# Kernel optimization log

Measured on AMD Instinct MI355X. Metric: run time of the kernel, lower is better.

Reference implementation:

```python
import jax, jax.numpy as jnp
import numpy as np


def _rmsnorm(x):
    # F.rms_norm with no weight, default eps = finfo(dtype).eps
    eps = jnp.asarray(jnp.finfo(x.dtype).eps, x.dtype)
    return x * jax.lax.rsqrt(jnp.mean(x * x, axis=-1, keepdims=True) + eps)


def _rope(x, cos, sin):
    d = x.shape[-1] // 2
    x1, x2 = x[..., :d], x[..., d:]
    return jnp.concatenate([x1 * cos + x2 * sin, -x1 * sin + x2 * cos], axis=-1)


def setup_inputs() -> dict:
    key = jax.random.key(0)
    ks = jax.random.split(key, 9)
    B, T, C, H, D = 4, 2048, 1024, 8, 128
    x = jax.random.normal(ks[0], (B, T, C), jnp.float32)
    ve = jax.random.normal(ks[1], (B, T, C), jnp.float32)
    cos = jax.random.uniform(ks[2], (1, T, 1, D // 2), jnp.float32)
    sin = jax.random.uniform(ks[3], (1, T, 1, D // 2), jnp.float32)
    s = 0.02
    Wq = jax.random.normal(ks[4], (C, C), jnp.float32) * s
    Wk = jax.random.normal(ks[5], (C, C), jnp.float32) * s
    Wv = jax.random.normal(ks[6], (C, C), jnp.float32) * s
    Wproj = jax.random.normal(ks[7], (C, C), jnp.float32) * s
    Wgate = jax.random.normal(ks[8], (H, 32), jnp.float32) * s
    return {"x": x, "ve": ve, "cos": cos, "sin": sin,
            "Wq": Wq, "Wk": Wk, "Wv": Wv, "Wproj": Wproj, "Wgate": Wgate,
            "window_size": 1024}


def reference(x, ve, cos, sin, Wq, Wk, Wv, Wproj, Wgate, window_size):
    B, T, C = x.shape
    H = Wgate.shape[0]
    D = C // H
    gate_ch = Wgate.shape[1]  # 32

    q = (x @ Wq.T).reshape(B, T, H, D)
    k = (x @ Wk.T).reshape(B, T, H, D)
    v = (x @ Wv.T).reshape(B, T, H, D)

    # value-embedding sigmoid gate: gate in (0, 2)
    gate = 2.0 * jax.nn.sigmoid(x[..., :gate_ch] @ Wgate.T)  # [B,T,H]
    v = v + gate[..., None] * ve.reshape(B, T, H, D)

    q = _rmsnorm(_rope(q, cos, sin))
    k = _rmsnorm(_rope(k, cos, sin))

    scale = jnp.asarray(D, q.dtype) ** -0.5
    scores = jnp.einsum("bqhd,bkhd->bhqk", q, k) * scale  # [B,H,T,T]

    pos = jnp.arange(T)
    row, col = pos[:, None], pos[None, :]
    mask = (col <= row) & (col >= row - window_size + 1)  # sliding causal window
    scores = jnp.where(mask, scores, -jnp.inf)
    attn = jax.nn.softmax(scores, axis=-1)

    y = jnp.einsum("bhqk,bkhd->bqhd", attn, v).reshape(B, T, C)
    return y @ Wproj.T
```

## Files before the change

### kernel.cpp

```cpp
#include <hip/hip_runtime.h>
#include <cstdint>
#include <cstddef>

typedef __bf16 bf16;
typedef __bf16 bf16x8 __attribute__((ext_vector_type(8)));
typedef float  f32x4  __attribute__((ext_vector_type(4)));

#define AS1 __attribute__((address_space(1)))
#define AS3 __attribute__((address_space(3)))

#define B_ 4
#define T_ 2048
#define C_ 1024
#define H_ 8
#define D_ 128
#define WIN_ 1024
#define PS_ 72

__global__ void cvt_kernel(const float* __restrict__ src, bf16* __restrict__ dst, int n) {
  int i = (blockIdx.x * 256 + threadIdx.x) * 8;
  if (i >= n) return;
  float4 a = *(const float4*)(src + i);
  float4 b = *(const float4*)(src + i + 4);
  bf16x8 o;
  o[0] = (bf16)a.x; o[1] = (bf16)a.y; o[2] = (bf16)a.z; o[3] = (bf16)a.w;
  o[4] = (bf16)b.x; o[5] = (bf16)b.y; o[6] = (bf16)b.z; o[7] = (bf16)b.w;
  *(bf16x8*)(dst + i) = o;
}

__device__ __forceinline__ void gemm_tile_compute(
    const bf16* __restrict__ A, const bf16* __restrict__ W,
    bf16* As, bf16* Bs, int m0, int n0, f32x4 acc[4][4])
{
  const int tid  = threadIdx.x;
  const int w    = tid >> 6;
  const int l    = tid & 63;
  const int quad = l >> 4;
  const int arow = l & 15;
  const int lrow = tid >> 3;
  const int lcol = ((tid & 7) ^ (lrow & 7)) * 8;
  const int wm = w >> 1, wn = w & 1;
  const int sw = (arow & 7);

  for (int kt = 0; kt < C_; kt += 64) {
    __syncthreads();
#pragma unroll
    for (int i = 0; i < 4; i++) {
      const bf16* ga = A + (size_t)(m0 + i * 32 + lrow) * C_ + kt + lcol;
      __builtin_amdgcn_global_load_lds((AS1 unsigned int*)ga,
          (AS3 unsigned int*)(As + i * 2048 + w * 512), 16, 0, 0);
      const bf16* gb = W + (size_t)(n0 + i * 32 + lrow) * C_ + kt + lcol;
      __builtin_amdgcn_global_load_lds((AS1 unsigned int*)gb,
          (AS3 unsigned int*)(Bs + i * 2048 + w * 512), 16, 0, 0);
    }
    __syncthreads();

#pragma unroll
    for (int ks = 0; ks < 2; ks++) {
      const int ch = ((ks * 4 + quad) ^ sw) * 8;
      bf16x8 af[4], bfr[4];
#pragma unroll
      for (int mt = 0; mt < 4; mt++)
        af[mt] = *(const bf16x8*)(As + (wm * 64 + mt * 16 + arow) * 64 + ch);
#pragma unroll
      for (int nt = 0; nt < 4; nt++)
        bfr[nt] = *(const bf16x8*)(Bs + (wn * 64 + nt * 16 + arow) * 64 + ch);
#pragma unroll
      for (int mt = 0; mt < 4; mt++)
#pragma unroll
        for (int nt = 0; nt < 4; nt++)
          acc[mt][nt] = __builtin_amdgcn_mfma_f32_16x16x32_bf16(af[mt], bfr[nt], acc[mt][nt], 0, 0, 0);
    }
  }
}

__global__ __launch_bounds__(256) void gemm_qkv(
    const bf16* __restrict__ xb, const bf16* __restrict__ wb,
    bf16* __restrict__ qh, bf16* __restrict__ kh, bf16* __restrict__ vh)
{
  __shared__ bf16 As[128 * 64];
  __shared__ bf16 Bs[128 * 64];
  const int z = blockIdx.z;
  const bf16* W = wb + (size_t)z * (C_ * C_);
  bf16* out = (z == 0) ? qh : (z == 1) ? kh : vh;
  const int m0 = blockIdx.y * 128, n0 = blockIdx.x * 128;

  f32x4 acc[4][4];
#pragma unroll
  for (int i = 0; i < 4; i++)
#pragma unroll
    for (int j = 0; j < 4; j++) acc[i][j] = (f32x4){0.f, 0.f, 0.f, 0.f};

  gemm_tile_compute(xb, W, As, Bs, m0, n0, acc);

  const int tid = threadIdx.x, w = tid >> 6, l = tid & 63;
  const int quad = l >> 4, lc = l & 15, wm = w >> 1, wn = w & 1;
#pragma unroll
  for (int mt = 0; mt < 4; mt++) {
#pragma unroll
    for (int nt = 0; nt < 4; nt++) {
      const int col = n0 + wn * 64 + nt * 16 + lc;
      const int h = col >> 7, d = col & 127;
#pragma unroll
      for (int r = 0; r < 4; r++) {
        const int row = m0 + wm * 64 + mt * 16 + quad * 4 + r;
        const int b = row >> 11, t = row & 2047;
        out[(((size_t)(b * H_ + h)) * T_ + t) * D_ + d] = (bf16)acc[mt][nt][r];
      }
    }
  }
}

__global__ __launch_bounds__(256) void gemm_proj(
    const bf16* __restrict__ yb, const bf16* __restrict__ wproj, float* __restrict__ out)
{
  __shared__ bf16 As[128 * 64];
  __shared__ bf16 Bs[128 * 64];
  const int m0 = blockIdx.y * 128, n0 = blockIdx.x * 128;

  f32x4 acc[4][4];
#pragma unroll
  for (int i = 0; i < 4; i++)
#pragma unroll
    for (int j = 0; j < 4; j++) acc[i][j] = (f32x4){0.f, 0.f, 0.f, 0.f};

  gemm_tile_compute(yb, wproj, As, Bs, m0, n0, acc);

  const int tid = threadIdx.x, w = tid >> 6, l = tid & 63;
  const int quad = l >> 4, lc = l & 15, wm = w >> 1, wn = w & 1;
#pragma unroll
  for (int mt = 0; mt < 4; mt++) {
#pragma unroll
    for (int nt = 0; nt < 4; nt++) {
      const int col = n0 + wn * 64 + nt * 16 + lc;
#pragma unroll
      for (int r = 0; r < 4; r++) {
        const int row = m0 + wm * 64 + mt * 16 + quad * 4 + r;
        out[(size_t)row * C_ + col] = acc[mt][nt][r];
      }
    }
  }
}

__global__ __launch_bounds__(256) void rope_rms_gate(
    bf16* __restrict__ qh, bf16* __restrict__ kh, bf16* __restrict__ vh,
    const float* __restrict__ x, const float* __restrict__ ve,
    const float* __restrict__ cosb, const float* __restrict__ sinb,
    const float* __restrict__ wg)
{
  const int tid = threadIdx.x, w = tid >> 6, l = tid & 63;
  const int rq = blockIdx.x * 4 + w;
  const int b = rq >> 14, h = (rq >> 11) & 7, t = rq & 2047;
  const float cv = cosb[t * 64 + l], sv = sinb[t * 64 + l];
  const float eps = 1.1920929e-07f;
  const float QSC = 0.08838834764831845f * 1.4426950408889634f;

  bf16* qr = qh + (size_t)rq * D_;
  float x1 = (float)qr[l], x2 = (float)qr[l + 64];
  float o1 = x1 * cv + x2 * sv;
  float o2 = x2 * cv - x1 * sv;
  float ss = o1 * o1 + o2 * o2;
#pragma unroll
  for (int off = 32; off; off >>= 1) ss += __shfl_xor(ss, off);
  float sc = rsqrtf(ss * (1.0f / 128.0f) + eps) * QSC;
  qr[l] = (bf16)(o1 * sc); qr[l + 64] = (bf16)(o2 * sc);

  bf16* kr = kh + (size_t)rq * D_;
  x1 = (float)kr[l]; x2 = (float)kr[l + 64];
  o1 = x1 * cv + x2 * sv;
  o2 = x2 * cv - x1 * sv;
  ss = o1 * o1 + o2 * o2;
#pragma unroll
  for (int off = 32; off; off >>= 1) ss += __shfl_xor(ss, off);
  sc = rsqrtf(ss * (1.0f / 128.0f) + eps);
  kr[l] = (bf16)(o1 * sc); kr[l + 64] = (bf16)(o2 * sc);

  const float* xr = x + ((size_t)(b * T_ + t)) * C_;
  float gp = (l < 32) ? xr[l] * wg[h * 32 + l] : 0.0f;
#pragma unroll
  for (int off = 32; off; off >>= 1) gp += __shfl_xor(gp, off);
  const float gate = 2.0f / (1.0f + __expf(-gp));
  bf16* vr = vh + (size_t)rq * D_;
  const float* ver = ve + ((size_t)(b * T_ + t)) * C_ + h * D_;
  vr[l]      = (bf16)((float)vr[l]      + gate * ver[l]);
  vr[l + 64] = (bf16)((float)vr[l + 64] + gate * ver[l + 64]);
}

__global__ __launch_bounds__(256) void transpose_v(
    const bf16* __restrict__ vh, bf16* __restrict__ vt)
{
  __shared__ float tile[64 * 65];
  const int bh = blockIdx.z;
  const int t0 = blockIdx.x * 64, d0 = blockIdx.y * 64;
  const int tid = threadIdx.x;
  const int r8 = tid >> 3, c8 = (tid & 7) * 8;
#pragma unroll
  for (int g = 0; g < 2; g++) {
    const int t = r8 + g * 32;
    bf16x8 v = *(const bf16x8*)(vh + ((size_t)bh * T_ + t0 + t) * D_ + d0 + c8);
#pragma unroll
    for (int j = 0; j < 8; j++) tile[t * 65 + c8 + j] = (float)v[j];
  }
  __syncthreads();
#pragma unroll
  for (int g = 0; g < 2; g++) {
    const int d = r8 + g * 32;
    bf16x8 o;
#pragma unroll
    for (int j = 0; j < 8; j++) o[j] = (bf16)tile[(c8 + j) * 65 + d];
    *(bf16x8*)(vt + ((size_t)bh * D_ + d0 + d) * T_ + t0 + c8) = o;
  }
}

__global__ __launch_bounds__(256) void attn_mfma(
    const bf16* __restrict__ qh, const bf16* __restrict__ kh,
    const bf16* __restrict__ vt, bf16* __restrict__ yb)
{
  __shared__ bf16 Ks[64 * 128];
  __shared__ bf16 VTs[128 * 64];
  __shared__ bf16 Ps[4 * 32 * PS_];
  const int bh = blockIdx.y;
  const int q0 = blockIdx.x * 128;
  const int tid = threadIdx.x;
  const int w = tid >> 6, l = tid & 63;
  const int quad = l >> 4, l15 = l & 15;
  const int sw = l15 & 7;
  const float FMAX = 16.5f;

  bf16x8 qf[2][4];
  const bf16* qbase = qh + ((size_t)bh * T_ + q0 + w * 32 + l15) * D_;
#pragma unroll
  for (int mt = 0; mt < 2; mt++)
#pragma unroll
    for (int dk = 0; dk < 4; dk++)
      qf[mt][dk] = *(const bf16x8*)(qbase + mt * 16 * D_ + dk * 32 + quad * 8);

  f32x4 O[2][8];
  f32x4 lst[2];
#pragma unroll
  for (int mt = 0; mt < 2; mt++) {
    lst[mt] = (f32x4){0.f, 0.f, 0.f, 0.f};
#pragma unroll
    for (int dn = 0; dn < 8; dn++) O[mt][dn] = (f32x4){0.f, 0.f, 0.f, 0.f};
  }

  const int kt_lo = (q0 >= WIN_) ? ((q0 - (WIN_ - 1)) >> 6) : 0;
  const int kt_hi = (q0 + 127) >> 6;
  const bf16* kg = kh + (size_t)bh * T_ * D_;
  const bf16* vg = vt + (size_t)bh * D_ * T_;
  bf16* Pw = Ps + w * 32 * PS_;

  const int krow_s = w * 4 + (l >> 4);
  const int kcol_s = (l15 ^ (krow_s & 7)) * 8;
  const int vrow_s = w * 8 + (l >> 3);
  const int vcol_s = (((l & 7) ^ (vrow_s & 7))) * 8;

  for (int kt = kt_lo; kt <= kt_hi; kt++) {
    const int k0 = kt * 64;
    __syncthreads();
#pragma unroll
    for (int s = 0; s < 4; s++) {
      const bf16* gk = kg + (size_t)(k0 + s * 16 + krow_s) * D_ + kcol_s;
      __builtin_amdgcn_global_load_lds((AS1 unsigned int*)gk,
          (AS3 unsigned int*)(Ks + s * 2048 + w * 512), 16, 0, 0);
      const bf16* gv = vg + (size_t)(s * 32 + vrow_s) * T_ + k0 + vcol_s;
      __builtin_amdgcn_global_load_lds((AS1 unsigned int*)gv,
          (AS3 unsigned int*)(VTs + s * 2048 + w * 512), 16, 0, 0);
    }
    __syncthreads();

    f32x4 sv[2][4];
#pragma unroll
    for (int mt = 0; mt < 2; mt++)
#pragma unroll
      for (int nf = 0; nf < 4; nf++) sv[mt][nf] = (f32x4){0.f, 0.f, 0.f, 0.f};
#pragma unroll
    for (int dk = 0; dk < 4; dk++) {
      const int ch = ((dk * 4 + quad) ^ sw) * 8;
      bf16x8 kf[4];
#pragma unroll
      for (int nf = 0; nf < 4; nf++)
        kf[nf] = *(const bf16x8*)(Ks + (nf * 16 + l15) * 128 + ch);
#pragma unroll
      for (int mt = 0; mt < 2; mt++)
#pragma unroll
        for (int nf = 0; nf < 4; nf++)
          sv[mt][nf] = __builtin_amdgcn_mfma_f32_16x16x32_bf16(qf[mt][dk], kf[nf], sv[mt][nf], 0, 0, 0);
    }

    if (!((k0 + 63 <= q0) && (k0 >= q0 + 128 - WIN_))) {
#pragma unroll
      for (int mt = 0; mt < 2; mt++)
#pragma unroll
        for (int nf = 0; nf < 4; nf++) {
          const int kcol = k0 + nf * 16 + l15;
#pragma unroll
          for (int r = 0; r < 4; r++) {
            const int qrow = q0 + w * 32 + mt * 16 + quad * 4 + r;
            const bool ok = (kcol <= qrow) && (kcol > qrow - WIN_);
            sv[mt][nf][r] = ok ? sv[mt][nf][r] : -3.0e38f;
          }
        }
    }

#pragma unroll
    for (int mt = 0; mt < 2; mt++) {
#pragma unroll
      for (int nf = 0; nf < 4; nf++)
#pragma unroll
        for (int r = 0; r < 4; r++) {
          const float p = __builtin_amdgcn_exp2f(sv[mt][nf][r] - FMAX);
          sv[mt][nf][r] = p;
          lst[mt][r] += p;
        }
#pragma unroll
      for (int nf = 0; nf < 4; nf++)
#pragma unroll
        for (int r = 0; r < 4; r++)
          Pw[(mt * 16 + quad * 4 + r) * PS_ + nf * 16 + l15] = (bf16)sv[mt][nf][r];
    }

    asm volatile("" ::: "memory");

#pragma unroll
    for (int ks = 0; ks < 2; ks++) {
      const int ch = ((ks * 4 + quad) ^ sw) * 8;
      bf16x8 af0 = *(const bf16x8*)(Pw + l15 * PS_ + ks * 32 + quad * 8);
      bf16x8 af1 = *(const bf16x8*)(Pw + (16 + l15) * PS_ + ks * 32 + quad * 8);
#pragma unroll
      for (int dn = 0; dn < 8; dn++) {
        bf16x8 bfv = *(const bf16x8*)(VTs + (dn * 16 + l15) * 64 + ch);
        O[0][dn] = __builtin_amdgcn_mfma_f32_16x16x32_bf16(af0, bfv, O[0][dn], 0, 0, 0);
        O[1][dn] = __builtin_amdgcn_mfma_f32_16x16x32_bf16(af1, bfv, O[1][dn], 0, 0, 0);
      }
    }
  }

#pragma unroll
  for (int mt = 0; mt < 2; mt++)
#pragma unroll
    for (int off = 1; off < 16; off <<= 1)
#pragma unroll
      for (int r = 0; r < 4; r++) lst[mt][r] += __shfl_xor(lst[mt][r], off);

  const int b = bh >> 3, h = bh & 7;
#pragma unroll
  for (int mt = 0; mt < 2; mt++) {
    f32x4 inv;
#pragma unroll
    for (int r = 0; r < 4; r++) inv[r] = 1.0f / lst[mt][r];
#pragma unroll
    for (int dn = 0; dn < 8; dn++)
#pragma unroll
      for (int r = 0; r < 4; r++) {
        const int t = q0 + w * 32 + mt * 16 + quad * 4 + r;
        yb[((size_t)(b * T_ + t)) * C_ + h * D_ + dn * 16 + l15] = (bf16)(O[mt][dn][r] * inv[r]);
      }
  }
}

extern "C" void kernel_launch(void* const* d_in, const int* in_sizes, int n_in,
                              void* d_out, int out_size, void* d_ws, size_t ws_size,
                              hipStream_t stream) {
  const float* x     = (const float*)d_in[0];
  const float* ve    = (const float*)d_in[1];
  const float* cosb  = (const float*)d_in[2];
  const float* sinb  = (const float*)d_in[3];
  const float* Wq    = (const float*)d_in[4];
  const float* Wk    = (const float*)d_in[5];
  const float* Wv    = (const float*)d_in[6];
  const float* Wproj = (const float*)d_in[7];
  const float* Wg    = (const float*)d_in[8];

  char* ws = (char*)d_ws;
  bf16* xb = (bf16*)ws;
  bf16* wb = (bf16*)(ws + 16777216);
  bf16* qh = (bf16*)(ws + 25165824);
  bf16* kh = (bf16*)(ws + 41943040);
  bf16* vh = (bf16*)(ws + 58720256);
  bf16* vtp = xb;
  bf16* yb = vh;

  const int NX = B_ * T_ * C_;
  const int NW = C_ * C_;

  cvt_kernel<<<NX / 8 / 256, 256, 0, stream>>>(x, xb, NX);
  cvt_kernel<<<NW / 8 / 256, 256, 0, stream>>>(Wq,    wb,          NW);
  cvt_kernel<<<NW / 8 / 256, 256, 0, stream>>>(Wk,    wb + NW,     NW);
  cvt_kernel<<<NW / 8 / 256, 256, 0, stream>>>(Wv,    wb + 2 * NW, NW);
  cvt_kernel<<<NW / 8 / 256, 256, 0, stream>>>(Wproj, wb + 3 * NW, NW);

  gemm_qkv<<<dim3(C_ / 128, (B_ * T_) / 128, 3), 256, 0, stream>>>(xb, wb, qh, kh, vh);
  rope_rms_gate<<<(B_ * H_ * T_) / 4, 256, 0, stream>>>(qh, kh, vh, x, ve, cosb, sinb, Wg);
  transpose_v<<<dim3(T_ / 64, D_ / 64, B_ * H_), 256, 0, stream>>>(vh, vtp);
  attn_mfma<<<dim3(T_ / 128, B_ * H_), 256, 0, stream>>>(qh, kh, vtp, yb);
  gemm_proj<<<dim3(C_ / 128, (B_ * T_) / 128), 256, 0, stream>>>(yb, wb + 3 * NW, (float*)d_out);
}
```

Before: 323.2 us.

## Fuse RoPE, RMSNorm, value gate and V-transpose into QKV GEMM epilogue, remap blocks per XCD

Moves the rope+rmsnorm for q/k, the sigmoid value-embedding gate add, and the V transpose into the QKV GEMM epilogue. The epilogue stages each tile through shared memory so it can write vectorized rows, and for V it writes the transposed layout directly. This removes two separate kernels and their round trips of q/k/v through global memory. It also merges the four weight conversions into one launch and flattens the grids with an XCD-aware block index mapping for the GEMMs and attention, aiming at better L2 locality. The cost is a larger epilogue with extra barriers and more shared memory in the GEMM.

New measurement: 356.8 us. +10.4%, slower.

```diff
diff --git a/kernel.cpp b/kernel.cpp
--- a/kernel.cpp
+++ b/kernel.cpp
@@ -16,6 +16,7 @@
 #define D_ 128
 #define WIN_ 1024
 #define PS_ 72
+#define TS_ 136
 
 __global__ void cvt_kernel(const float* __restrict__ src, bf16* __restrict__ dst, int n) {
   int i = (blockIdx.x * 256 + threadIdx.x) * 8;
@@ -26,6 +27,20 @@
   o[0] = (bf16)a.x; o[1] = (bf16)a.y; o[2] = (bf16)a.z; o[3] = (bf16)a.w;
   o[4] = (bf16)b.x; o[5] = (bf16)b.y; o[6] = (bf16)b.z; o[7] = (bf16)b.w;
   *(bf16x8*)(dst + i) = o;
+}
+
+__global__ void cvt_w4(const float* __restrict__ w0, const float* __restrict__ w1,
+                       const float* __restrict__ w2, const float* __restrict__ w3,
+                       bf16* __restrict__ dst) {
+  const int z = blockIdx.y;
+  const float* src = (z == 0) ? w0 : (z == 1) ? w1 : (z == 2) ? w2 : w3;
+  int i = (blockIdx.x * 256 + threadIdx.x) * 8;
+  float4 a = *(const float4*)(src + i);
+  float4 b = *(const float4*)(src + i + 4);
+  bf16x8 o;
+  o[0] = (bf16)a.x; o[1] = (bf16)a.y; o[2] = (bf16)a.z; o[3] = (bf16)a.w;
+  o[4] = (bf16)b.x; o[5] = (bf16)b.y; o[6] = (bf16)b.z; o[7] = (bf16)b.w;
+  *(bf16x8*)(dst + (size_t)z * (C_ * C_) + i) = o;
 }
 
 __device__ __forceinline__ void gemm_tile_compute(
@@ -76,15 +91,24 @@
 
 __global__ __launch_bounds__(256) void gemm_qkv(
     const bf16* __restrict__ xb, const bf16* __restrict__ wb,
-    bf16* __restrict__ qh, bf16* __restrict__ kh, bf16* __restrict__ vh)
+    const float* __restrict__ x, const float* __restrict__ ve,
+    const float* __restrict__ cosb, const float* __restrict__ sinb,
+    const float* __restrict__ wg,
+    bf16* __restrict__ qh, bf16* __restrict__ kh, bf16* __restrict__ vt)
 {
-  __shared__ bf16 As[128 * 64];
-  __shared__ bf16 Bs[128 * 64];
-  const int z = blockIdx.z;
+  __shared__ bf16 TileS[128 * TS_];
+  __shared__ float Gs[128];
+  bf16* As = TileS;
+  bf16* Bs = TileS + 8192;
+
+  const int bid = blockIdx.x;
+  const int xcd = bid & 7, local = bid >> 3;
+  const int mi = local / 24, rem = local % 24;
+  const int z = rem >> 3, n = rem & 7;
+  const int m = mi * 8 + xcd;
+  const int m0 = m * 128, n0 = n * 128, h = n;
+
   const bf16* W = wb + (size_t)z * (C_ * C_);
-  bf16* out = (z == 0) ? qh : (z == 1) ? kh : vh;
-  const int m0 = blockIdx.y * 128, n0 = blockIdx.x * 128;
-
   f32x4 acc[4][4];
 #pragma unroll
   for (int i = 0; i < 4; i++)
@@ -94,19 +118,113 @@
   gemm_tile_compute(xb, W, As, Bs, m0, n0, acc);
 
   const int tid = threadIdx.x, w = tid >> 6, l = tid & 63;
-  const int quad = l >> 4, lc = l & 15, wm = w >> 1, wn = w & 1;
-#pragma unroll
-  for (int mt = 0; mt < 4; mt++) {
-#pragma unroll
-    for (int nt = 0; nt < 4; nt++) {
-      const int col = n0 + wn * 64 + nt * 16 + lc;
-      const int h = col >> 7, d = col & 127;
-#pragma unroll
-      for (int r = 0; r < 4; r++) {
-        const int row = m0 + wm * 64 + mt * 16 + quad * 4 + r;
-        const int b = row >> 11, t = row & 2047;
-        out[(((size_t)(b * H_ + h)) * T_ + t) * D_ + d] = (bf16)acc[mt][nt][r];
+  const int quad = l >> 4, l15 = l & 15, wm = w >> 1, wn = w & 1;
+  const int bb = m0 >> 11;
+  const int tbase = m0 & 2047;
+
+  if (z == 2) {
+    {
+      const int r = tid >> 1, p = tid & 1;
+      const float* xr = x + ((size_t)(bb * T_ + tbase + r)) * C_ + p * 16;
+      const float* wgr = wg + h * 32 + p * 16;
+      float partial = 0.f;
+#pragma unroll
+      for (int j = 0; j < 16; j++) partial += xr[j] * wgr[j];
+      partial += __shfl_xor(partial, 1);
+      if (p == 0) Gs[r] = 2.0f / (1.0f + __expf(-partial));
+    }
+    __syncthreads();
+
+#pragma unroll
+    for (int mt = 0; mt < 4; mt++)
+#pragma unroll
+      for (int nt = 0; nt < 4; nt++) {
+        const int col = wn * 64 + nt * 16 + l15;
+#pragma unroll
+        for (int r = 0; r < 4; r++) {
+          const int rowl = wm * 64 + mt * 16 + quad * 4 + r;
+          const float vv = acc[mt][nt][r]
+              + Gs[rowl] * ve[((size_t)(bb * T_ + tbase + rowl)) * C_ + h * D_ + col];
+          TileS[col * TS_ + rowl] = (bf16)vv;
+        }
       }
+    __syncthreads();
+
+    const int dr = tid >> 1, p = tid & 1;
+    bf16* outp = vt + (((size_t)(bb * H_ + h)) * D_ + dr) * T_ + tbase + p * 64;
+#pragma unroll
+    for (int c = 0; c < 8; c++)
+      *(bf16x8*)(outp + c * 8) = *(const bf16x8*)(TileS + dr * TS_ + p * 64 + c * 8);
+  } else {
+    __syncthreads();
+#pragma unroll
+    for (int mt = 0; mt < 4; mt++)
+#pragma unroll
+      for (int nt = 0; nt < 4; nt++) {
+        const int col = wn * 64 + nt * 16 + l15;
+#pragma unroll
+        for (int r = 0; r < 4; r++) {
+          const int rowl = wm * 64 + mt * 16 + quad * 4 + r;
+          TileS[rowl * TS_ + col] = (bf16)acc[mt][nt][r];
+        }
+      }
+    __syncthreads();
+
+    const int r = tid >> 1, p = tid & 1;
+    const int t = tbase + r;
+    const float QSC = 0.08838834764831845f * 1.4426950408889634f;
+    const float eps = 1.1920929e-07f;
+    const float4* cp = (const float4*)(cosb + (size_t)t * 64 + p * 32);
+    const float4* sp = (const float4*)(sinb + (size_t)t * 64 + p * 32);
+    const bf16* t1 = TileS + r * TS_ + p * 32;
+    const bf16* t2 = t1 + 64;
+
+    float ss = 0.f;
+#pragma unroll
+    for (int c = 0; c < 8; c++) {
+      float4 cv = cp[c], sv = sp[c];
+      const bf16* a = t1 + c * 4;
+      const bf16* bq = t2 + c * 4;
+      float x1, x2, o1, o2;
+      x1 = (float)a[0]; x2 = (float)bq[0];
+      o1 = x1 * cv.x + x2 * sv.x; o2 = x2 * cv.x - x1 * sv.x; ss += o1 * o1 + o2 * o2;
+      x1 = (float)a[1]; x2 = (float)bq[1];
+      o1 = x1 * cv.y + x2 * sv.y; o2 = x2 * cv.y - x1 * sv.y; ss += o1 * o1 + o2 * o2;
+      x1 = (float)a[2]; x2 = (float)bq[2];
+      o1 = x1 * cv.z + x2 * sv.z; o2 = x2 * cv.z - x1 * sv.z; ss += o1 * o1 + o2 * o2;
+      x1 = (float)a[3]; x2 = (float)bq[3];
+      o1 = x1 * cv.w + x2 * sv.w; o2 = x2 * cv.w - x1 * sv.w; ss += o1 * o1 + o2 * o2;
+    }
+    ss += __shfl_xor(ss, 1);
+    const float sc = rsqrtf(ss * (1.0f / 128.0f) + eps) * (z == 0 ? QSC : 1.0f);
+
+    bf16* outp = (z == 0 ? qh : kh) + (((size_t)(bb * H_ + h)) * T_ + t) * D_ + p * 32;
+#pragma unroll
+    for (int c = 0; c < 4; c++) {
+      float4 cv = cp[c * 2], cv2 = cp[c * 2 + 1];
+      float4 sv = sp[c * 2], sv2 = sp[c * 2 + 1];
+      const bf16* a = t1 + c * 8;
+      const bf16* bq = t2 + c * 8;
+      bf16x8 o1v, o2v;
+      float x1, x2;
+      x1 = (float)a[0]; x2 = (float)bq[0];
+      o1v[0] = (bf16)((x1 * cv.x + x2 * sv.x) * sc); o2v[0] = (bf16)((x2 * cv.x - x1 * sv.x) * sc);
+      x1 = (float)a[1]; x2 = (float)bq[1];
+      o1v[1] = (bf16)((x1 * cv.y + x2 * sv.y) * sc); o2v[1] = (bf16)((x2 * cv.y - x1 * sv.y) * sc);
+      x1 = (float)a[2]; x2 = (float)bq[2];
+      o1v[2] = (bf16)((x1 * cv.z + x2 * sv.z) * sc); o2v[2] = (bf16)((x2 * cv.z - x1 * sv.z) * sc);
+      x1 = (float)a[3]; x2 = (float)bq[3];
+      o1v[3] = (bf16)((x1 * cv.w + x2 * sv.w) * sc); o2v[3] = (bf16)((x2 * cv.w - x1 * sv.w) * sc);
+      x1 = (float)a[4]; x2 = (float)bq[4];
+      o1v[4] = (bf16)((x1 * cv2.x + x2 * sv2.x) * sc); o2v[4] = (bf16)((x2 * cv2.x - x1 * sv2.x) * sc);
+      x1 = (float)a[5]; x2 = (float)bq[5];
+      o1v[5] = (bf16)((x1 * cv2.y + x2 * sv2.y) * sc); o2v[5] = (bf16)((x2 * cv2.y - x1 * sv2.y) * sc);
+      x1 = (float)a[6]; x2 = (float)bq[6];
+      o1v[6] = (bf16)((x1 * cv2.z + x2 * sv2.z) * sc); o2v[6] = (bf16)((x2 * cv2.z - x1 * sv2.z) * sc);
+      x1 = (float)a[7]; x2 = (float)bq[7];
+      o1v[7] = (bf16)((x1 * cv2.w + x2 * sv2.w) * sc); o2v[7] = (bf16)((x2 * cv2.w - x1 * sv2.w) * sc);
+      *(bf16x8*)(outp + c * 8) = o1v;
+      *(bf16x8*)(outp + 64 + c * 8) = o2v;
     }
   }
 }
@@ -116,7 +234,10 @@
 {
   __shared__ bf16 As[128 * 64];
   __shared__ bf16 Bs[128 * 64];
-  const int m0 = blockIdx.y * 128, n0 = blockIdx.x * 128;
+  const int bid = blockIdx.x;
+  const int xcd = bid & 7, local = bid >> 3;
+  const int m = xcd * 8 + (local >> 3), n = local & 7;
+  const int m0 = m * 128, n0 = n * 128;
 
   f32x4 acc[4][4];
 #pragma unroll
@@ -139,76 +260,6 @@
         out[(size_t)row * C_ + col] = acc[mt][nt][r];
       }
     }
-  }
-}
-
-__global__ __launch_bounds__(256) void rope_rms_gate(
-    bf16* __restrict__ qh, bf16* __restrict__ kh, bf16* __restrict__ vh,
-    const float* __restrict__ x, const float* __restrict__ ve,
-    const float* __restrict__ cosb, const float* __restrict__ sinb,
-    const float* __restrict__ wg)
-{
-  const int tid = threadIdx.x, w = tid >> 6, l = tid & 63;
-  const int rq = blockIdx.x * 4 + w;
-  const int b = rq >> 14, h = (rq >> 11) & 7, t = rq & 2047;
-  const float cv = cosb[t * 64 + l], sv = sinb[t * 64 + l];
-  const float eps = 1.1920929e-07f;
-  const float QSC = 0.08838834764831845f * 1.4426950408889634f;
-
-  bf16* qr = qh + (size_t)rq * D_;
-  float x1 = (float)qr[l], x2 = (float)qr[l + 64];
-  float o1 = x1 * cv + x2 * sv;
-  float o2 = x2 * cv - x1 * sv;
-  float ss = o1 * o1 + o2 * o2;
-#pragma unroll
-  for (int off = 32; off; off >>= 1) ss += __shfl_xor(ss, off);
-  float sc = rsqrtf(ss * (1.0f / 128.0f) + eps) * QSC;
-  qr[l] = (bf16)(o1 * sc); qr[l + 64] = (bf16)(o2 * sc);
-
-  bf16* kr = kh + (size_t)rq * D_;
-  x1 = (float)kr[l]; x2 = (float)kr[l + 64];
-  o1 = x1 * cv + x2 * sv;
-  o2 = x2 * cv - x1 * sv;
-  ss = o1 * o1 + o2 * o2;
-#pragma unroll
-  for (int off = 32; off; off >>= 1) ss += __shfl_xor(ss, off);
-  sc = rsqrtf(ss * (1.0f / 128.0f) + eps);
-  kr[l] = (bf16)(o1 * sc); kr[l + 64] = (bf16)(o2 * sc);
-
-  const float* xr = x + ((size_t)(b * T_ + t)) * C_;
-  float gp = (l < 32) ? xr[l] * wg[h * 32 + l] : 0.0f;
-#pragma unroll
-  for (int off = 32; off; off >>= 1) gp += __shfl_xor(gp, off);
-  const float gate = 2.0f / (1.0f + __expf(-gp));
-  bf16* vr = vh + (size_t)rq * D_;
-  const float* ver = ve + ((size_t)(b * T_ + t)) * C_ + h * D_;
-  vr[l]      = (bf16)((float)vr[l]      + gate * ver[l]);
-  vr[l + 64] = (bf16)((float)vr[l + 64] + gate * ver[l + 64]);
-}
-
-__global__ __launch_bounds__(256) void transpose_v(
-    const bf16* __restrict__ vh, bf16* __restrict__ vt)
-{
-  __shared__ float tile[64 * 65];
-  const int bh = blockIdx.z;
-  const int t0 = blockIdx.x * 64, d0 = blockIdx.y * 64;
-  const int tid = threadIdx.x;
-  const int r8 = tid >> 3, c8 = (tid & 7) * 8;
-#pragma unroll
-  for (int g = 0; g < 2; g++) {
-    const int t = r8 + g * 32;
-    bf16x8 v = *(const bf16x8*)(vh + ((size_t)bh * T_ + t0 + t) * D_ + d0 + c8);
-#pragma unroll
-    for (int j = 0; j < 8; j++) tile[t * 65 + c8 + j] = (float)v[j];
-  }
-  __syncthreads();
-#pragma unroll
-  for (int g = 0; g < 2; g++) {
-    const int d = r8 + g * 32;
-    bf16x8 o;
-#pragma unroll
-    for (int j = 0; j < 8; j++) o[j] = (bf16)tile[(c8 + j) * 65 + d];
-    *(bf16x8*)(vt + ((size_t)bh * D_ + d0 + d) * T_ + t0 + c8) = o;
   }
 }
 
@@ -219,8 +270,10 @@
   __shared__ bf16 Ks[64 * 128];
   __shared__ bf16 VTs[128 * 64];
   __shared__ bf16 Ps[4 * 32 * PS_];
-  const int bh = blockIdx.y;
-  const int q0 = blockIdx.x * 128;
+  const int bid = blockIdx.x;
+  const int xcd = bid & 7, local = bid >> 3;
+  const int bh = xcd * 4 + (local >> 4);
+  const int q0 = (local & 15) * 128;
   const int tid = threadIdx.x;
   const int w = tid >> 6, l = tid & 63;
   const int quad = l >> 4, l15 = l & 15;
@@ -377,22 +430,16 @@
   bf16* wb = (bf16*)(ws + 16777216);
   bf16* qh = (bf16*)(ws + 25165824);
   bf16* kh = (bf16*)(ws + 41943040);
-  bf16* vh = (bf16*)(ws + 58720256);
-  bf16* vtp = xb;
-  bf16* yb = vh;
+  bf16* vt = (bf16*)(ws + 58720256);
+  bf16* yb = xb;
 
   const int NX = B_ * T_ * C_;
   const int NW = C_ * C_;
 
   cvt_kernel<<<NX / 8 / 256, 256, 0, stream>>>(x, xb, NX);
-  cvt_kernel<<<NW / 8 / 256, 256, 0, stream>>>(Wq,    wb,          NW);
-  cvt_kernel<<<NW / 8 / 256, 256, 0, stream>>>(Wk,    wb + NW,     NW);
-  cvt_kernel<<<NW / 8 / 256, 256, 0, stream>>>(Wv,    wb + 2 * NW, NW);
-  cvt_kernel<<<NW / 8 / 256, 256, 0, stream>>>(Wproj, wb + 3 * NW, NW);
-
-  gemm_qkv<<<dim3(C_ / 128, (B_ * T_) / 128, 3), 256, 0, stream>>>(xb, wb, qh, kh, vh);
-  rope_rms_gate<<<(B_ * H_ * T_) / 4, 256, 0, stream>>>(qh, kh, vh, x, ve, cosb, sinb, Wg);
-  transpose_v<<<dim3(T_ / 64, D_ / 64, B_ * H_), 256, 0, stream>>>(vh, vtp);
-  attn_mfma<<<dim3(T_ / 128, B_ * H_), 256, 0, stream>>>(qh, kh, vtp, yb);
-  gemm_proj<<<dim3(C_ / 128, (B_ * T_) / 128), 256, 0, stream>>>(yb, wb + 3 * NW, (float*)d_out);
-}
+  cvt_w4<<<dim3(NW / 8 / 256, 4), 256, 0, stream>>>(Wq, Wk, Wv, Wproj, wb);
+
+  gemm_qkv<<<1536, 256, 0, stream>>>(xb, wb, x, ve, cosb, sinb, Wg, qh, kh, vt);
+  attn_mfma<<<512, 256, 0, stream>>>(qh, kh, vt, yb);
+  gemm_proj<<<512, 256, 0, stream>>>(yb, wb + 3 * NW, (float*)d_out);
+}
```

## Fuse rope/gate with V transpose, batch weight casts, remap attention blocks per XCD

Applied to the files above, without the earlier changes.

Merges the four weight-conversion launches into one 2D-grid kernel. Fuses the RoPE+RMSNorm+gate kernel with the V transpose, so gated V goes through shared memory and is written straight to the transposed layout, with vectorized 16-element-per-thread loads. Remaps the attention grid to 1D so consecutive blocks on the same XCD share a head, aiming for better L2 reuse of K/V. The cost is more shared memory per block in the fused kernel and a hardcoded block-to-XCD mapping.

Result: faster. 299.2 us (-7.4%).

```diff
diff --git a/kernel.cpp b/kernel.cpp
--- a/kernel.cpp
+++ b/kernel.cpp
@@ -26,6 +26,20 @@
   o[0] = (bf16)a.x; o[1] = (bf16)a.y; o[2] = (bf16)a.z; o[3] = (bf16)a.w;
   o[4] = (bf16)b.x; o[5] = (bf16)b.y; o[6] = (bf16)b.z; o[7] = (bf16)b.w;
   *(bf16x8*)(dst + i) = o;
+}
+
+__global__ void cvt_w4(const float* __restrict__ w0, const float* __restrict__ w1,
+                       const float* __restrict__ w2, const float* __restrict__ w3,
+                       bf16* __restrict__ dst) {
+  const int z = blockIdx.y;
+  const float* src = (z == 0) ? w0 : (z == 1) ? w1 : (z == 2) ? w2 : w3;
+  int i = (blockIdx.x * 256 + threadIdx.x) * 8;
+  float4 a = *(const float4*)(src + i);
+  float4 b = *(const float4*)(src + i + 4);
+  bf16x8 o;
+  o[0] = (bf16)a.x; o[1] = (bf16)a.y; o[2] = (bf16)a.z; o[3] = (bf16)a.w;
+  o[4] = (bf16)b.x; o[5] = (bf16)b.y; o[6] = (bf16)b.z; o[7] = (bf16)b.w;
+  *(bf16x8*)(dst + (size_t)z * (C_ * C_) + i) = o;
 }
 
 __device__ __forceinline__ void gemm_tile_compute(
@@ -142,73 +156,107 @@
   }
 }
 
-__global__ __launch_bounds__(256) void rope_rms_gate(
-    bf16* __restrict__ qh, bf16* __restrict__ kh, bf16* __restrict__ vh,
+__global__ __launch_bounds__(256) void rope_gate_t(
+    bf16* __restrict__ qh, bf16* __restrict__ kh, const bf16* __restrict__ vh,
     const float* __restrict__ x, const float* __restrict__ ve,
     const float* __restrict__ cosb, const float* __restrict__ sinb,
-    const float* __restrict__ wg)
+    const float* __restrict__ wg, bf16* __restrict__ vt)
 {
-  const int tid = threadIdx.x, w = tid >> 6, l = tid & 63;
-  const int rq = blockIdx.x * 4 + w;
-  const int b = rq >> 14, h = (rq >> 11) & 7, t = rq & 2047;
-  const float cv = cosb[t * 64 + l], sv = sinb[t * 64 + l];
+  __shared__ float Tile[64 * 129];
+  __shared__ float Gs[64];
+  const int bh = blockIdx.y;
+  const int t0 = blockIdx.x * 64;
+  const int b = bh >> 3, h = bh & 7;
+  const int tid = threadIdx.x;
+  const int r = tid >> 2, p = tid & 3;
+  const int t = t0 + r;
   const float eps = 1.1920929e-07f;
   const float QSC = 0.08838834764831845f * 1.4426950408889634f;
 
-  bf16* qr = qh + (size_t)rq * D_;
-  float x1 = (float)qr[l], x2 = (float)qr[l + 64];
-  float o1 = x1 * cv + x2 * sv;
-  float o2 = x2 * cv - x1 * sv;
-  float ss = o1 * o1 + o2 * o2;
-#pragma unroll
-  for (int off = 32; off; off >>= 1) ss += __shfl_xor(ss, off);
-  float sc = rsqrtf(ss * (1.0f / 128.0f) + eps) * QSC;
-  qr[l] = (bf16)(o1 * sc); qr[l + 64] = (bf16)(o2 * sc);
-
-  bf16* kr = kh + (size_t)rq * D_;
-  x1 = (float)kr[l]; x2 = (float)kr[l + 64];
-  o1 = x1 * cv + x2 * sv;
-  o2 = x2 * cv - x1 * sv;
-  ss = o1 * o1 + o2 * o2;
-#pragma unroll
-  for (int off = 32; off; off >>= 1) ss += __shfl_xor(ss, off);
-  sc = rsqrtf(ss * (1.0f / 128.0f) + eps);
-  kr[l] = (bf16)(o1 * sc); kr[l + 64] = (bf16)(o2 * sc);
-
-  const float* xr = x + ((size_t)(b * T_ + t)) * C_;
-  float gp = (l < 32) ? xr[l] * wg[h * 32 + l] : 0.0f;
-#pragma unroll
-  for (int off = 32; off; off >>= 1) gp += __shfl_xor(gp, off);
-  const float gate = 2.0f / (1.0f + __expf(-gp));
-  bf16* vr = vh + (size_t)rq * D_;
-  const float* ver = ve + ((size_t)(b * T_ + t)) * C_ + h * D_;
-  vr[l]      = (bf16)((float)vr[l]      + gate * ver[l]);
-  vr[l + 64] = (bf16)((float)vr[l + 64] + gate * ver[l + 64]);
-}
-
-__global__ __launch_bounds__(256) void transpose_v(
-    const bf16* __restrict__ vh, bf16* __restrict__ vt)
-{
-  __shared__ float tile[64 * 65];
-  const int bh = blockIdx.z;
-  const int t0 = blockIdx.x * 64, d0 = blockIdx.y * 64;
-  const int tid = threadIdx.x;
-  const int r8 = tid >> 3, c8 = (tid & 7) * 8;
-#pragma unroll
-  for (int g = 0; g < 2; g++) {
-    const int t = r8 + g * 32;
-    bf16x8 v = *(const bf16x8*)(vh + ((size_t)bh * T_ + t0 + t) * D_ + d0 + c8);
-#pragma unroll
-    for (int j = 0; j < 8; j++) tile[t * 65 + c8 + j] = (float)v[j];
-  }
+  {
+    const float* xr = x + ((size_t)(b * T_ + t)) * C_ + p * 8;
+    const float* wgr = wg + h * 32 + p * 8;
+    float gp = 0.f;
+#pragma unroll
+    for (int j = 0; j < 8; j++) gp += xr[j] * wgr[j];
+    gp += __shfl_xor(gp, 1);
+    gp += __shfl_xor(gp, 2);
+    if (p == 0) Gs[r] = 2.0f / (1.0f + __expf(-gp));
+  }
+
+  const float4* cp = (const float4*)(cosb + (size_t)t * 64 + p * 16);
+  const float4* sp = (const float4*)(sinb + (size_t)t * 64 + p * 16);
+#pragma unroll
+  for (int zz = 0; zz < 2; zz++) {
+    bf16* rowp = (zz == 0 ? qh : kh) + ((size_t)bh * T_ + t) * D_ + p * 16;
+    bf16x8 a0 = *(const bf16x8*)(rowp);
+    bf16x8 a1 = *(const bf16x8*)(rowp + 8);
+    bf16x8 b0 = *(const bf16x8*)(rowp + 64);
+    bf16x8 b1 = *(const bf16x8*)(rowp + 72);
+    float o1[16], o2[16];
+    float ss = 0.f;
+#pragma unroll
+    for (int c = 0; c < 4; c++) {
+      float4 cv = cp[c], sv = sp[c];
+      float cf[4] = {cv.x, cv.y, cv.z, cv.w};
+      float sf[4] = {sv.x, sv.y, sv.z, sv.w};
+#pragma unroll
+      for (int j = 0; j < 4; j++) {
+        const int e = c * 4 + j;
+        const float x1 = (float)(e < 8 ? a0[e] : a1[e - 8]);
+        const float x2 = (float)(e < 8 ? b0[e] : b1[e - 8]);
+        o1[e] = x1 * cf[j] + x2 * sf[j];
+        o2[e] = x2 * cf[j] - x1 * sf[j];
+        ss += o1[e] * o1[e] + o2[e] * o2[e];
+      }
+    }
+    ss += __shfl_xor(ss, 1);
+    ss += __shfl_xor(ss, 2);
+    const float sc = rsqrtf(ss * (1.0f / 128.0f) + eps) * (zz == 0 ? QSC : 1.0f);
+    bf16x8 w0, w1, w2, w3;
+#pragma unroll
+    for (int e = 0; e < 8; e++) {
+      w0[e] = (bf16)(o1[e] * sc); w1[e] = (bf16)(o1[e + 8] * sc);
+      w2[e] = (bf16)(o2[e] * sc); w3[e] = (bf16)(o2[e + 8] * sc);
+    }
+    *(bf16x8*)(rowp) = w0; *(bf16x8*)(rowp + 8) = w1;
+    *(bf16x8*)(rowp + 64) = w2; *(bf16x8*)(rowp + 72) = w3;
+  }
+
   __syncthreads();
-#pragma unroll
-  for (int g = 0; g < 2; g++) {
-    const int d = r8 + g * 32;
-    bf16x8 o;
-#pragma unroll
-    for (int j = 0; j < 8; j++) o[j] = (bf16)tile[(c8 + j) * 65 + d];
-    *(bf16x8*)(vt + ((size_t)bh * D_ + d0 + d) * T_ + t0 + c8) = o;
+  {
+    const float g = Gs[r];
+    const bf16* vr = vh + ((size_t)bh * T_ + t) * D_ + p * 32;
+    const float* ver = ve + ((size_t)(b * T_ + t)) * C_ + h * D_ + p * 32;
+    float* tr = Tile + r * 129 + p * 32;
+#pragma unroll
+    for (int c = 0; c < 4; c++) {
+      bf16x8 vv = *(const bf16x8*)(vr + c * 8);
+      float4 e0 = *(const float4*)(ver + c * 8);
+      float4 e1 = *(const float4*)(ver + c * 8 + 4);
+      tr[c * 8 + 0] = (float)vv[0] + g * e0.x;
+      tr[c * 8 + 1] = (float)vv[1] + g * e0.y;
+      tr[c * 8 + 2] = (float)vv[2] + g * e0.z;
+      tr[c * 8 + 3] = (float)vv[3] + g * e0.w;
+      tr[c * 8 + 4] = (float)vv[4] + g * e1.x;
+      tr[c * 8 + 5] = (float)vv[5] + g * e1.y;
+      tr[c * 8 + 6] = (float)vv[6] + g * e1.z;
+      tr[c * 8 + 7] = (float)vv[7] + g * e1.w;
+    }
+  }
+  __syncthreads();
+
+  {
+    const int d = tid >> 1, half = tid & 1;
+    bf16* outp = vt + (((size_t)bh) * D_ + d) * T_ + t0 + half * 32;
+#pragma unroll
+    for (int c = 0; c < 4; c++) {
+      bf16x8 o;
+#pragma unroll
+      for (int j = 0; j < 8; j++)
+        o[j] = (bf16)Tile[(half * 32 + c * 8 + j) * 129 + d];
+      *(bf16x8*)(outp + c * 8) = o;
+    }
   }
 }
 
@@ -219,8 +267,10 @@
   __shared__ bf16 Ks[64 * 128];
   __shared__ bf16 VTs[128 * 64];
   __shared__ bf16 Ps[4 * 32 * PS_];
-  const int bh = blockIdx.y;
-  const int q0 = blockIdx.x * 128;
+  const int bid = blockIdx.x;
+  const int xcd = bid & 7, local = bid >> 3;
+  const int bh = xcd * 4 + (local >> 4);
+  const int q0 = (local & 15) * 128;
   const int tid = threadIdx.x;
   const int w = tid >> 6, l = tid & 63;
   const int quad = l >> 4, l15 = l & 15;
@@ -378,21 +428,17 @@
   bf16* qh = (bf16*)(ws + 25165824);
   bf16* kh = (bf16*)(ws + 41943040);
   bf16* vh = (bf16*)(ws + 58720256);
-  bf16* vtp = xb;
+  bf16* vt = xb;
   bf16* yb = vh;
 
   const int NX = B_ * T_ * C_;
   const int NW = C_ * C_;
 
   cvt_kernel<<<NX / 8 / 256, 256, 0, stream>>>(x, xb, NX);
-  cvt_kernel<<<NW / 8 / 256, 256, 0, stream>>>(Wq,    wb,          NW);
-  cvt_kernel<<<NW / 8 / 256, 256, 0, stream>>>(Wk,    wb + NW,     NW);
-  cvt_kernel<<<NW / 8 / 256, 256, 0, stream>>>(Wv,    wb + 2 * NW, NW);
-  cvt_kernel<<<NW / 8 / 256, 256, 0, stream>>>(Wproj, wb + 3 * NW, NW);
+  cvt_w4<<<dim3(NW / 8 / 256, 4), 256, 0, stream>>>(Wq, Wk, Wv, Wproj, wb);
 
   gemm_qkv<<<dim3(C_ / 128, (B_ * T_) / 128, 3), 256, 0, stream>>>(xb, wb, qh, kh, vh);
-  rope_rms_gate<<<(B_ * H_ * T_) / 4, 256, 0, stream>>>(qh, kh, vh, x, ve, cosb, sinb, Wg);
-  transpose_v<<<dim3(T_ / 64, D_ / 64, B_ * H_), 256, 0, stream>>>(vh, vtp);
-  attn_mfma<<<dim3(T_ / 128, B_ * H_), 256, 0, stream>>>(qh, kh, vtp, yb);
+  rope_gate_t<<<dim3(T_ / 64, B_ * H_), 256, 0, stream>>>(qh, kh, vh, x, ve, cosb, sinb, Wg, vt);
+  attn_mfma<<<512, 256, 0, stream>>>(qh, kh, vt, yb);
   gemm_proj<<<dim3(C_ / 128, (B_ * T_) / 128), 256, 0, stream>>>(yb, wb + 3 * NW, (float*)d_out);
 }
```
